# Optimization experiments

Measured on AMD Instinct MI355X. Metric: run time of the kernel, lower is better.

Reference implementation:

```python
import jax, jax.numpy as jnp
import numpy as np

B, S, V, D, H, C, NH = 8, 512, 32000, 768, 768, 9, 8
DH = D // NH


def setup_inputs() -> dict:
    key = jax.random.key(0)
    ks = list(jax.random.split(key, 24))
    it = iter(ks)

    def w(shape, s=0.02):
        return jax.random.normal(next(it), shape, jnp.float32) * s

    return {
        "input_ids": jax.random.randint(next(it), (B, S), 0, V, dtype=jnp.int32),
        "labels": jax.random.randint(next(it), (B, S), 0, C, dtype=jnp.int32),
        "emb_table": w((V, D), 1.0),
        "hw_Wh": w((D, D)),
        "hw_bh": jnp.zeros((D,), jnp.float32),
        "hw_Wt": w((D, D)),
        "hw_bt": jnp.zeros((D,), jnp.float32),
        "in_proj_w": w((3 * D, D)),
        "in_proj_b": jnp.zeros((3 * D,), jnp.float32),
        "out_proj_w": w((D, D)),
        "out_proj_b": jnp.zeros((D,), jnp.float32),
        "lstm0_Wih": w((2, 4 * H, D)),
        "lstm0_Whh": w((2, 4 * H, H)),
        "lstm0_b": jnp.zeros((2, 4 * H), jnp.float32),
        "lstm1_Wih": w((2, 4 * H, 2 * H)),
        "lstm1_Whh": w((2, 4 * H, H)),
        "lstm1_b": jnp.zeros((2, 4 * H), jnp.float32),
        "fc_W": w((C, 2 * H)),
        "fc_b": jnp.zeros((C,), jnp.float32),
        "crf_start": w((C,), 0.1),
        "crf_end": w((C,), 0.1),
        "crf_trans": w((C, C), 0.1),
    }


def _lstm_dir(x, Wih, Whh, b, reverse):
    # x: [B,S,in] -> outputs [B,S,H]; PyTorch gate order i,f,g,o
    xt = x.transpose(1, 0, 2)  # [S,B,in]
    h0 = jnp.zeros((x.shape[0], H), x.dtype)

    def step(carry, xt_):
        h, c = carry
        g = xt_ @ Wih.T + h @ Whh.T + b
        i, f, gg, o = jnp.split(g, 4, axis=-1)
        c = jax.nn.sigmoid(f) * c + jax.nn.sigmoid(i) * jnp.tanh(gg)
        h = jax.nn.sigmoid(o) * jnp.tanh(c)
        return (h, c), h

    _, hs = jax.lax.scan(step, (h0, h0), xt, reverse=reverse)
    return hs.transpose(1, 0, 2)


def _bilstm_layer(x, Wih, Whh, b):
    fwd = _lstm_dir(x, Wih[0], Whh[0], b[0], False)
    bwd = _lstm_dir(x, Wih[1], Whh[1], b[1], True)
    return jnp.concatenate([fwd, bwd], axis=-1)


def _emissions(input_ids, emb_table, hw_Wh, hw_bh, hw_Wt, hw_bt,
               in_proj_w, in_proj_b, out_proj_w, out_proj_b,
               lstm0_Wih, lstm0_Whh, lstm0_b, lstm1_Wih, lstm1_Whh, lstm1_b,
               fc_W, fc_b):
    x = emb_table[input_ids]  # [B,S,D]
    # Highway (1 layer, relu)
    hh = jax.nn.relu(x @ hw_Wh.T + hw_bh)
    t = jax.nn.sigmoid(x @ hw_Wt.T + hw_bt)
    x = t * hh + (1.0 - t) * x
    # Multi-head self-attention
    qkv = x @ in_proj_w.T + in_proj_b
    q, k, v = jnp.split(qkv, 3, axis=-1)
    hd = lambda a: a.reshape(B, S, NH, DH).transpose(0, 2, 1, 3)  # [B,NH,S,DH]
    q, k, v = hd(q), hd(k), hd(v)
    att = jax.nn.softmax(jnp.einsum('bhqd,bhkd->bhqk', q, k) / np.float32(np.sqrt(DH)), axis=-1)
    o = jnp.einsum('bhqk,bhkd->bhqd', att, v).transpose(0, 2, 1, 3).reshape(B, S, D)
    x = o @ out_proj_w.T + out_proj_b
    # 2-layer BiLSTM (inference: dropout off)
    x = _bilstm_layer(x, lstm0_Wih, lstm0_Whh, lstm0_b)
    x = _bilstm_layer(x, lstm1_Wih, lstm1_Whh, lstm1_b)
    return x @ fc_W.T + fc_b  # [B,S,C]


def _crf_nll(emissions, tags, crf_start, crf_end, crf_trans):
    # full mask (labels==-100 replaced by 0 before mask built), reduction='sum'
    em_t = emissions.transpose(1, 0, 2)  # [S,B,C]
    num = crf_start[tags[:, 0]] + crf_end[tags[:, -1]]
    num = num + jnp.take_along_axis(emissions, tags[..., None], axis=-1)[..., 0].sum(-1)
    num = num + crf_trans[tags[:, :-1], tags[:, 1:]].sum(-1)
    a0 = crf_start + em_t[0]  # [B,C]

    def fstep(a, em):
        a = jax.scipy.special.logsumexp(a[:, :, None] + crf_trans[None], axis=1) + em
        return a, None

    aT, _ = jax.lax.scan(fstep, a0, em_t[1:])
    logZ = jax.scipy.special.logsumexp(aT + crf_end, axis=-1)
    return -(num - logZ).sum()


def _viterbi(emissions, crf_start, crf_end, crf_trans):
    em_t = emissions.transpose(1, 0, 2)  # [S,B,C]
    s0 = crf_start + em_t[0]

    def vstep(s, em):
        sc = s[:, :, None] + crf_trans[None]  # [B,C_prev,C_next]
        return jnp.max(sc, axis=1) + em, jnp.argmax(sc, axis=1)

    sT, bps = jax.lax.scan(vstep, s0, em_t[1:])  # bps: [S-1,B,C]
    last = jnp.argmax(sT + crf_end, axis=-1)  # [B]

    def bstep(tag, bp):
        prev = jnp.take_along_axis(bp, tag[:, None], axis=1)[:, 0]
        return prev, prev

    _, path = jax.lax.scan(bstep, last, bps, reverse=True)  # [S-1,B]
    return jnp.concatenate([path, last[None]], axis=0).transpose(1, 0)  # [B,S]


def reference(input_ids, labels, emb_table, hw_Wh, hw_bh, hw_Wt, hw_bt,
              in_proj_w, in_proj_b, out_proj_w, out_proj_b,
              lstm0_Wih, lstm0_Whh, lstm0_b, lstm1_Wih, lstm1_Whh, lstm1_b,
              fc_W, fc_b, crf_start, crf_end, crf_trans):
    emissions = _emissions(input_ids, emb_table, hw_Wh, hw_bh, hw_Wt, hw_bt,
                           in_proj_w, in_proj_b, out_proj_w, out_proj_b,
                           lstm0_Wih, lstm0_Whh, lstm0_b,
                           lstm1_Wih, lstm1_Whh, lstm1_b, fc_W, fc_b)
    loss = _crf_nll(emissions, labels, crf_start, crf_end, crf_trans)
    decode = _viterbi(emissions, crf_start, crf_end, crf_trans)
    return loss, decode
```

## Files before the change

### kernel.cpp

```cpp
#include <hip/hip_runtime.h>
#include <cstdint>

#define B_   8
#define S_   512
#define D_   768
#define C_   9
#define BS_  4096

typedef unsigned long long u64;

__global__ __launch_bounds__(192) void k_embed(const int* __restrict__ ids,
                                               const float* __restrict__ emb,
                                               float* __restrict__ x) {
  int row = blockIdx.x;
  int id = ids[row];
  const float4* src = (const float4*)(emb + (size_t)id * D_);
  float4* dst = (float4*)(x + (size_t)row * D_);
  dst[threadIdx.x] = src[threadIdx.x];
}

#define GIDX(k, m) ((k)*144 + (m) + (((m) >> 5) << 2))

__global__ __launch_bounds__(256) void k_gemm(const float* __restrict__ A,
                                              const float* __restrict__ W,
                                              const float* __restrict__ bias,
                                              float* __restrict__ C,
                                              int M, int N, int K, int act, int mode) {
  __shared__ float As[2304];
  __shared__ float Bs[2304];
  int nwg = gridDim.x * gridDim.y;
  int lin = blockIdx.y * gridDim.x + blockIdx.x;
  int cpx = nwg >> 3;
  int swz = (lin & 7) * cpx + (lin >> 3);
  int bxs = swz % gridDim.x, bys = swz / gridDim.x;
  int bm0 = bys * 128, bn0 = bxs * 128;
  int tid = threadIdx.x;
  int tm = tid >> 4, tn = tid & 15;
  float acc[8][8];
#pragma unroll
  for (int i = 0; i < 8; ++i)
#pragma unroll
    for (int j = 0; j < 8; ++j) acc[i][j] = 0.f;

  for (int k0 = 0; k0 < K; k0 += 16) {
    __syncthreads();
#pragma unroll
    for (int j = 0; j < 2; ++j) {
      int f4 = tid + j * 256;
      int r = f4 >> 2;
      int kq = (f4 & 3) * 4;
      float4 va = *(const float4*)(A + (size_t)(bm0 + r) * K + k0 + kq);
      As[GIDX(kq + 0, r)] = va.x; As[GIDX(kq + 1, r)] = va.y;
      As[GIDX(kq + 2, r)] = va.z; As[GIDX(kq + 3, r)] = va.w;
      float4 vb = *(const float4*)(W + (size_t)(bn0 + r) * K + k0 + kq);
      Bs[GIDX(kq + 0, r)] = vb.x; Bs[GIDX(kq + 1, r)] = vb.y;
      Bs[GIDX(kq + 2, r)] = vb.z; Bs[GIDX(kq + 3, r)] = vb.w;
    }
    __syncthreads();
#pragma unroll
    for (int kk = 0; kk < 16; ++kk) {
      float a[8], b[8];
      *(float4*)&a[0] = *(const float4*)&As[GIDX(kk, tm * 8)];
      *(float4*)&a[4] = *(const float4*)&As[GIDX(kk, tm * 8 + 4)];
      *(float4*)&b[0] = *(const float4*)&Bs[GIDX(kk, tn * 8)];
      *(float4*)&b[4] = *(const float4*)&Bs[GIDX(kk, tn * 8 + 4)];
#pragma unroll
      for (int i = 0; i < 8; ++i)
#pragma unroll
        for (int j = 0; j < 8; ++j) acc[i][j] += a[i] * b[j];
    }
  }

  float bv[8];
#pragma unroll
  for (int j = 0; j < 8; ++j) bv[j] = bias[bn0 + tn * 8 + j];
#pragma unroll
  for (int i = 0; i < 8; ++i) {
    int row = bm0 + tm * 8 + i;
    float o[8];
#pragma unroll
    for (int j = 0; j < 8; ++j) {
      float v = acc[i][j] + bv[j];
      if (act == 1) v = fmaxf(v, 0.f);
      else if (act == 2) v = 1.f / (1.f + expf(-v));
      o[j] = v;
    }
    if (mode == 0) {
      float* cp = C + (size_t)row * N + bn0 + tn * 8;
      *(float4*)cp = make_float4(o[0], o[1], o[2], o[3]);
      *(float4*)(cp + 4) = make_float4(o[4], o[5], o[6], o[7]);
    } else {
      int bb = row >> 9, t = row & 511;
#pragma unroll
      for (int j = 0; j < 8; ++j) {
        unsigned n = bn0 + tn * 8 + j;
        unsigned dir = n / 3072u;
        unsigned n2 = n - dir * 3072u;
        unsigned g = n2 / 768u;
        unsigned rem = n2 - g * 768u;
        unsigned grp = rem >> 3, u = rem & 7;
        C[(((size_t)(dir * 512 + t) * 96 + grp) << 8) + u * 32 + g * 8 + bb] = o[j];
      }
    }
  }
}

__global__ __launch_bounds__(256) void k_highway(float* __restrict__ x,
                                                 const float* __restrict__ hh,
                                                 const float* __restrict__ tt) {
  const int n4 = BS_ * D_ / 4;
  for (int i = blockIdx.x * 256 + threadIdx.x; i < n4; i += gridDim.x * 256) {
    float4 xv = ((const float4*)x)[i];
    float4 hv = ((const float4*)hh)[i];
    float4 tv = ((const float4*)tt)[i];
    xv.x = tv.x * hv.x + (1.f - tv.x) * xv.x;
    xv.y = tv.y * hv.y + (1.f - tv.y) * xv.y;
    xv.z = tv.z * hv.z + (1.f - tv.z) * xv.z;
    xv.w = tv.w * hv.w + (1.f - tv.w) * xv.w;
    ((float4*)x)[i] = xv;
  }
}

__global__ __launch_bounds__(256) void k_attn(const float* __restrict__ qkv,
                                              float* __restrict__ out) {
  __shared__ float Qs[16 * 100];
  __shared__ float Ks[32 * 101];
  __shared__ float Ps[16 * 513];
  int bh = blockIdx.x;
  int b = bh >> 3, h = bh & 7;
  int q0 = blockIdx.y * 16;
  int tid = threadIdx.x;
  const float scale = 0.10206207261596577f;

  const float* qb = qkv + (size_t)(b * 512 + q0) * 2304 + h * 96;
  for (int i = tid; i < 16 * 96; i += 256) {
    int r = i / 96, c = i - r * 96;
    Qs[r * 100 + c] = qb[(size_t)r * 2304 + c];
  }
  int qi = tid >> 4, kseg = tid & 15;

  for (int kt = 0; kt < 16; ++kt) {
    __syncthreads();
    const float* kb = qkv + (size_t)(b * 512 + kt * 32) * 2304 + 768 + h * 96;
    for (int i = tid; i < 32 * 96; i += 256) {
      int r = i / 96, c = i - r * 96;
      Ks[r * 101 + c] = kb[(size_t)r * 2304 + c];
    }
    __syncthreads();
    int kj0 = kseg * 2;
    float s0 = 0.f, s1 = 0.f;
    const float* qrow = &Qs[qi * 100];
    const float* k0p = &Ks[kj0 * 101];
    const float* k1p = &Ks[(kj0 + 1) * 101];
#pragma unroll 8
    for (int d = 0; d < 96; ++d) {
      float qv = qrow[d];
      s0 += qv * k0p[d];
      s1 += qv * k1p[d];
    }
    Ps[qi * 513 + kt * 32 + kj0] = s0 * scale;
    Ps[qi * 513 + kt * 32 + kj0 + 1] = s1 * scale;
  }
  __syncthreads();

  {
    float m = -1e30f;
    for (int j = 0; j < 32; ++j) m = fmaxf(m, Ps[qi * 513 + kseg + j * 16]);
    m = fmaxf(m, __shfl_xor(m, 1)); m = fmaxf(m, __shfl_xor(m, 2));
    m = fmaxf(m, __shfl_xor(m, 4)); m = fmaxf(m, __shfl_xor(m, 8));
    float sum = 0.f;
    for (int j = 0; j < 32; ++j) {
      int idx = qi * 513 + kseg + j * 16;
      float e = expf(Ps[idx] - m);
      Ps[idx] = e;
      sum += e;
    }
    sum += __shfl_xor(sum, 1); sum += __shfl_xor(sum, 2);
    sum += __shfl_xor(sum, 4); sum += __shfl_xor(sum, 8);
    float inv = 1.f / sum;
    for (int j = 0; j < 32; ++j) Ps[qi * 513 + kseg + j * 16] *= inv;
  }

  float acc[6] = {0.f, 0.f, 0.f, 0.f, 0.f, 0.f};
  int d0 = kseg * 6;
  for (int kt = 0; kt < 16; ++kt) {
    __syncthreads();
    const float* vb = qkv + (size_t)(b * 512 + kt * 32) * 2304 + 1536 + h * 96;
    for (int i = tid; i < 32 * 96; i += 256) {
      int r = i / 96, c = i - r * 96;
      Ks[r * 101 + c] = vb[(size_t)r * 2304 + c];
    }
    __syncthreads();
#pragma unroll 4
    for (int kj = 0; kj < 32; ++kj) {
      float p = Ps[qi * 513 + kt * 32 + kj];
      const float* vrow = &Ks[kj * 101 + d0];
#pragma unroll
      for (int u = 0; u < 6; ++u) acc[u] += p * vrow[u];
    }
  }
  float* ob = out + (size_t)(b * 512 + q0 + qi) * 768 + h * 96 + d0;
#pragma unroll
  for (int u = 0; u < 6; ++u) ob[u] = acc[u];
}

#define NWGD 96
__global__ __launch_bounds__(256, 1) void k_lstm(const float* __restrict__ gates,
                                                 const float* __restrict__ Whh,
                                                 float* __restrict__ hbuf,
                                                 float* __restrict__ hs,
                                                 int* __restrict__ flags) {
  __shared__ float hlds[8 * 772];
  int tid = threadIdx.x;
  int wg = blockIdx.x;
  int dir = wg / NWGD;
  int grp = wg % NWGD;
  int rg = tid >> 5;
  int ks = tid & 31;

  float4 w4[4][6];
#pragma unroll
  for (int j = 0; j < 4; ++j) {
    const float* wp = Whh + ((size_t)dir * 3072 + j * 768 + grp * 8 + rg) * 768 + ks * 4;
#pragma unroll
    for (int jj = 0; jj < 6; ++jj)
      w4[j][jj] = *(const float4*)(wp + jj * 128);
  }

  float* hb = hbuf + (size_t)dir * 2 * 6144;
  const float* gbase = gates + (size_t)dir * 512 * 24576 + grp * 256 + tid;
  const float* hp = hlds + ks * 4;
  float cst = 0.f;

  for (int step = 0; step < 512; ++step) {
    int t = dir ? (511 - step) : step;
    float gqv = gbase[(size_t)t * 24576];

#pragma unroll
    for (int i = 0; i < 3; ++i) {
      int idx = i * 256 + tid;
      int b2 = idx / 96;
      int kq = (idx - b2 * 96) * 8;
      const u64* src = (const u64*)(hb + (step & 1) * 6144 + b2 * 768 + kq);
      u64 lo  = __hip_atomic_load(src + 0, __ATOMIC_RELAXED, __HIP_MEMORY_SCOPE_AGENT);
      u64 hi  = __hip_atomic_load(src + 1, __ATOMIC_RELAXED, __HIP_MEMORY_SCOPE_AGENT);
      u64 lo2 = __hip_atomic_load(src + 2, __ATOMIC_RELAXED, __HIP_MEMORY_SCOPE_AGENT);
      u64 hi2 = __hip_atomic_load(src + 3, __ATOMIC_RELAXED, __HIP_MEMORY_SCOPE_AGENT);
      float* dst = &hlds[b2 * 772 + kq];
      *(u64*)(dst + 0) = lo;
      *(u64*)(dst + 2) = hi;
      *(u64*)(dst + 4) = lo2;
      *(u64*)(dst + 6) = hi2;
    }
    __syncthreads();

    float v[32];
#pragma unroll
    for (int i = 0; i < 32; ++i) v[i] = 0.f;
#pragma unroll
    for (int jj = 0; jj < 6; ++jj) {
#pragma unroll
      for (int b2 = 0; b2 < 8; ++b2) {
        float4 hv = *(const float4*)(hp + b2 * 772 + jj * 128);
#pragma unroll
        for (int j = 0; j < 4; ++j) {
          float4 w = w4[j][jj];
          v[j * 8 + b2] = fmaf(w.x, hv.x, v[j * 8 + b2]);
          v[j * 8 + b2] = fmaf(w.y, hv.y, v[j * 8 + b2]);
          v[j * 8 + b2] = fmaf(w.z, hv.z, v[j * 8 + b2]);
          v[j * 8 + b2] = fmaf(w.w, hv.w, v[j * 8 + b2]);
        }
      }
    }

    {
      bool hi = (ks & 16) != 0;
#pragma unroll
      for (int i = 0; i < 16; ++i) {
        float keep = hi ? v[i + 16] : v[i];
        float send = hi ? v[i] : v[i + 16];
        v[i] = keep + __shfl_xor(send, 16);
      }
    }
    {
      bool hi = (ks & 8) != 0;
#pragma unroll
      for (int i = 0; i < 8; ++i) {
        float keep = hi ? v[i + 8] : v[i];
        float send = hi ? v[i] : v[i + 8];
        v[i] = keep + __shfl_xor(send, 8);
      }
    }
    {
      bool hi = (ks & 4) != 0;
#pragma unroll
      for (int i = 0; i < 4; ++i) {
        float keep = hi ? v[i + 4] : v[i];
        float send = hi ? v[i] : v[i + 4];
        v[i] = keep + __shfl_xor(send, 4);
      }
    }
    {
      bool hi = (ks & 2) != 0;
#pragma unroll
      for (int i = 0; i < 2; ++i) {
        float keep = hi ? v[i + 2] : v[i];
        float send = hi ? v[i] : v[i + 2];
        v[i] = keep + __shfl_xor(send, 2);
      }
    }
    {
      bool hi = (ks & 1) != 0;
      float keep = hi ? v[1] : v[0];
      float send = hi ? v[0] : v[1];
      v[0] = keep + __shfl_xor(send, 1);
    }

    float gv = v[0] + gqv;
    float gf = __shfl_down(gv, 8);
    float gg = __shfl_down(gv, 16);
    float go = __shfl_down(gv, 24);
    float hnew = 0.f;
    if (ks < 8) {
      float i_ = 1.f / (1.f + expf(-gv));
      float f_ = 1.f / (1.f + expf(-gf));
      float ci = tanhf(gg);
      float o_ = 1.f / (1.f + expf(-go));
      cst = f_ * cst + i_ * ci;
      hnew = o_ * tanhf(cst);
      __hip_atomic_store(hb + (size_t)((step + 1) & 1) * 6144 + ks * 768 + grp * 8 + rg,
                         hnew, __ATOMIC_RELAXED, __HIP_MEMORY_SCOPE_AGENT);
    }

    __syncthreads();
    if (tid == 0)
      __hip_atomic_store(&flags[wg * 32], step + 1, __ATOMIC_RELAXED, __HIP_MEMORY_SCOPE_AGENT);
    if (ks < 8)
      hs[((size_t)(ks * 512 + t)) * 1536 + dir * 768 + grp * 8 + rg] = hnew;
    if (tid < NWGD) {
      const int* fp = &flags[(dir * NWGD + tid) * 32];
      while (__hip_atomic_load(fp, __ATOMIC_RELAXED, __HIP_MEMORY_SCOPE_AGENT) <= step)
        __builtin_amdgcn_s_sleep(2);
    }
    __syncthreads();
  }
}

__global__ __launch_bounds__(256) void k_fc(const float* __restrict__ A,
                                            const float* __restrict__ Wf,
                                            const float* __restrict__ bf,
                                            float* __restrict__ out) {
  __shared__ float Wl[9 * 1536];
  int tid = threadIdx.x;
  for (int i = tid; i < 9 * 1536; i += 256) Wl[i] = Wf[i];
  __syncthreads();
  int lane = tid & 63, wv = tid >> 6;
  int row = blockIdx.x * 4 + wv;
  const float* a = A + (size_t)row * 1536;
  float acc[9];
#pragma unroll
  for (int c = 0; c < 9; ++c) acc[c] = 0.f;
  for (int i = 0; i < 24; ++i) {
    float av = a[lane + i * 64];
#pragma unroll
    for (int c = 0; c < 9; ++c) acc[c] += av * Wl[c * 1536 + lane + i * 64];
  }
#pragma unroll
  for (int c = 0; c < 9; ++c) {
#pragma unroll
    for (int m = 1; m < 64; m <<= 1) acc[c] += __shfl_xor(acc[c], m);
  }
  if (lane == 0) {
#pragma unroll
    for (int c = 0; c < 9; ++c) out[(size_t)row * 9 + c] = acc[c] + bf[c];
  }
}

__global__ __launch_bounds__(512) void k_crf(const float* __restrict__ em,
                                             const int* __restrict__ labels,
                                             const float* __restrict__ cs,
                                             const float* __restrict__ ce,
                                             const float* __restrict__ ct,
                                             float* __restrict__ out) {
  __shared__ float trans_s[81];
  __shared__ unsigned char bps[8][511][12];
  __shared__ float partres[16];
  int tid = threadIdx.x;
  int b = tid >> 6;
  int lane = tid & 63;
  bool act = lane < 9;
  if (tid < 81) trans_s[tid] = ct[tid];
  __syncthreads();

  float tcol[9];
#pragma unroll
  for (int cp = 0; cp < 9; ++cp) tcol[cp] = act ? trans_s[cp * 9 + lane] : 0.f;

  float a_ = -1e30f, v_ = -1e30f;
  if (act) {
    float e0 = em[((size_t)b * 512) * 9 + lane];
    a_ = cs[lane] + e0;
    v_ = a_;
  }

  float e = act ? em[((size_t)b * 512 + 1) * 9 + lane] : 0.f;
  for (int t = 1; t < 512; ++t) {
    float e_nxt = 0.f;
    if (act && t < 511) e_nxt = em[((size_t)b * 512 + t + 1) * 9 + lane];
    float m = -1e30f, vm = -1e30f;
    int bp = 0;
    float xs[9];
#pragma unroll
    for (int cp = 0; cp < 9; ++cp) {
      float ap = __shfl(a_, cp);
      float vp = __shfl(v_, cp);
      float x = ap + tcol[cp];
      xs[cp] = x;
      m = fmaxf(m, x);
      float y = vp + tcol[cp];
      if (y > vm) { vm = y; bp = cp; }
    }
    float ssum = 0.f;
#pragma unroll
    for (int cp = 0; cp < 9; ++cp) ssum += expf(xs[cp] - m);
    if (act) {
      a_ = m + logf(ssum) + e;
      v_ = vm + e;
      bps[b][t - 1][lane] = (unsigned char)bp;
    }
    e = e_nxt;
  }

  float fin = act ? a_ + ce[lane] : -1e30f;
  float vfin = act ? v_ + ce[lane] : -1e30f;
  float m2 = fin;
  m2 = fmaxf(m2, __shfl_xor(m2, 1)); m2 = fmaxf(m2, __shfl_xor(m2, 2));
  m2 = fmaxf(m2, __shfl_xor(m2, 4)); m2 = fmaxf(m2, __shfl_xor(m2, 8));
  float s2 = expf(fin - m2);
  s2 += __shfl_xor(s2, 1); s2 += __shfl_xor(s2, 2);
  s2 += __shfl_xor(s2, 4); s2 += __shfl_xor(s2, 8);
  float logZ = m2 + logf(s2);

  float bv = vfin; int bi = lane;
#pragma unroll
  for (int s = 1; s < 16; s <<= 1) {
    float ov = __shfl_xor(bv, s);
    int oi = __shfl_xor(bi, s);
    if (ov > bv || (ov == bv && oi < bi)) { bv = ov; bi = oi; }
  }

  float np = 0.f;
  for (int t = lane; t < 512; t += 64) {
    int tg = labels[b * 512 + t];
    np += em[((size_t)b * 512 + t) * 9 + tg];
    if (t < 511) np += trans_s[tg * 9 + labels[b * 512 + t + 1]];
  }
#pragma unroll
  for (int s = 1; s < 64; s <<= 1) np += __shfl_xor(np, s);

  if (lane == 0) {
    np += cs[labels[b * 512]] + ce[labels[b * 512 + 511]];
    partres[b] = np;
    partres[8 + b] = logZ;
    out[1 + b * 512 + 511] = (float)bi;
    int tg = bi;
    for (int t = 510; t >= 0; --t) {
      tg = bps[b][t][tg];
      out[1 + b * 512 + t] = (float)tg;
    }
  }
  __syncthreads();
  if (tid == 0) {
    float acc = 0.f;
#pragma unroll
    for (int b2 = 0; b2 < 8; ++b2) acc += partres[b2] - partres[8 + b2];
    out[0] = -acc;
  }
}

extern "C" void kernel_launch(void* const* d_in, const int* in_sizes, int n_in,
                              void* d_out, int out_size, void* d_ws, size_t ws_size,
                              hipStream_t stream) {
  (void)in_sizes; (void)n_in; (void)out_size; (void)ws_size;
  const int*   ids    = (const int*)d_in[0];
  const int*   labels = (const int*)d_in[1];
  const float* emb    = (const float*)d_in[2];
  const float* hwWh   = (const float*)d_in[3];
  const float* hwbh   = (const float*)d_in[4];
  const float* hwWt   = (const float*)d_in[5];
  const float* hwbt   = (const float*)d_in[6];
  const float* ipw    = (const float*)d_in[7];
  const float* ipb    = (const float*)d_in[8];
  const float* opw    = (const float*)d_in[9];
  const float* opb    = (const float*)d_in[10];
  const float* l0Wih  = (const float*)d_in[11];
  const float* l0Whh  = (const float*)d_in[12];
  const float* l0b    = (const float*)d_in[13];
  const float* l1Wih  = (const float*)d_in[14];
  const float* l1Whh  = (const float*)d_in[15];
  const float* l1b    = (const float*)d_in[16];
  const float* fcW    = (const float*)d_in[17];
  const float* fcb    = (const float*)d_in[18];
  const float* cs     = (const float*)d_in[19];
  const float* ce     = (const float*)d_in[20];
  const float* ct     = (const float*)d_in[21];

  float* ws   = (float*)d_ws;
  float* x0   = ws;
  float* gbuf = ws + 3145728;
  float* hh   = gbuf;
  float* tt   = gbuf + 3145728;
  float* qkv  = gbuf + 6291456;
  float* x1   = ws + 28311552;
  float* hs0  = ws + 31457280;
  float* hs1  = ws + 37748736;
  float* em   = ws + 44040192;
  float* hbuf = ws + 44077056;
  int*   flags = (int*)(ws + 44101632);

  dim3 g768(6, 32), g2304(18, 32), g6144(48, 32);

  k_embed<<<BS_, 192, 0, stream>>>(ids, emb, x0);
  k_gemm<<<g768, 256, 0, stream>>>(x0, hwWh, hwbh, hh, BS_, 768, 768, 1, 0);
  k_gemm<<<g768, 256, 0, stream>>>(x0, hwWt, hwbt, tt, BS_, 768, 768, 2, 0);
  k_highway<<<768, 256, 0, stream>>>(x0, hh, tt);
  k_gemm<<<g2304, 256, 0, stream>>>(x0, ipw, ipb, qkv, BS_, 2304, 768, 0, 0);
  k_attn<<<dim3(64, 32), 256, 0, stream>>>(qkv, x0);
  k_gemm<<<g768, 256, 0, stream>>>(x0, opw, opb, x1, BS_, 768, 768, 0, 0);

  k_gemm<<<g6144, 256, 0, stream>>>(x1, l0Wih, l0b, gbuf, BS_, 6144, 768, 0, 1);
  hipMemsetAsync(hbuf, 0, (24576 + 192 * 32) * sizeof(float), stream);
  k_lstm<<<192, 256, 0, stream>>>(gbuf, l0Whh, hbuf, hs0, flags);

  k_gemm<<<g6144, 256, 0, stream>>>(hs0, l1Wih, l1b, gbuf, BS_, 6144, 1536, 0, 1);
  hipMemsetAsync(hbuf, 0, (24576 + 192 * 32) * sizeof(float), stream);
  k_lstm<<<192, 256, 0, stream>>>(gbuf, l1Whh, hbuf, hs1, flags);

  k_fc<<<1024, 256, 0, stream>>>(hs1, fcW, fcb, em);
  k_crf<<<1, 512, 0, stream>>>(em, labels, cs, ce, ct, (float*)d_out);
}
```

Baseline: 8.094 ms.

## Compute LSTM input-gate GEMMs with split-bf16 MFMA instead of FP32 SIMT

Activations and weights are converted into interleaved hi/lo bf16 planes, so a bf16 MFMA GEMM over 3K (hi*hi, hi*lo, lo*hi) approximates FP32 products for both LSTM input projections. The output is scattered into the same gate layout the recurrence kernel expects. The aim is to replace slow FP32 FMA throughput with matrix-core throughput. In exchange it adds conversion passes and extra workspace, and it depends on the workspace being large enough; otherwise it falls back to the old kernel.

```diff
diff --git a/kernel.cpp b/kernel.cpp
--- a/kernel.cpp
+++ b/kernel.cpp
@@ -1,4 +1,5 @@
 #include <hip/hip_runtime.h>
+#include <hip/hip_bf16.h>
 #include <cstdint>
 
 #define B_   8
@@ -8,6 +9,9 @@
 #define BS_  4096
 
 typedef unsigned long long u64;
+typedef unsigned short ushort_t;
+typedef short bf16x8 __attribute__((ext_vector_type(8)));
+typedef float f32x4 __attribute__((ext_vector_type(4)));
 
 __global__ __launch_bounds__(192) void k_embed(const int* __restrict__ ids,
                                                const float* __restrict__ emb,
@@ -105,6 +109,110 @@
   }
 }
 
+__device__ inline ushort_t f2bf_bits(float x) {
+  __hip_bfloat16 h = __float2bfloat16(x);
+  return __builtin_bit_cast(ushort_t, h);
+}
+__device__ inline float bf2f(ushort_t b) {
+  return __bfloat162float(__builtin_bit_cast(__hip_bfloat16, b));
+}
+
+__global__ __launch_bounds__(256) void k_cvt(const float* __restrict__ src,
+                                             ushort_t* __restrict__ dst,
+                                             int K, int total4, int mode) {
+  int kq4 = K >> 2;
+  for (int idx = blockIdx.x * 256 + threadIdx.x; idx < total4; idx += gridDim.x * 256) {
+    int m = idx / kq4;
+    int kq = (idx - m * kq4) * 4;
+    float4 v = *(const float4*)(src + (size_t)m * K + kq);
+    ushort4 hi, lo;
+    hi.x = f2bf_bits(v.x); lo.x = f2bf_bits(v.x - bf2f(hi.x));
+    hi.y = f2bf_bits(v.y); lo.y = f2bf_bits(v.y - bf2f(hi.y));
+    hi.z = f2bf_bits(v.z); lo.z = f2bf_bits(v.z - bf2f(hi.z));
+    hi.w = f2bf_bits(v.w); lo.w = f2bf_bits(v.w - bf2f(hi.w));
+    ushort_t* base = dst + (size_t)m * 3 * K + kq;
+    *(ushort4*)(base)         = hi;
+    *(ushort4*)(base + K)     = mode ? hi : lo;
+    *(ushort4*)(base + 2 * K) = mode ? lo : hi;
+  }
+}
+
+__global__ __launch_bounds__(256) void k_gates16(const ushort_t* __restrict__ A,
+                                                 const ushort_t* __restrict__ W,
+                                                 const float* __restrict__ bias,
+                                                 float* __restrict__ C,
+                                                 int Kp) {
+  __shared__ ushort_t Asb[128 * 64];
+  __shared__ ushort_t Bsb[128 * 64];
+  int nwg = gridDim.x * gridDim.y;
+  int lin = blockIdx.y * gridDim.x + blockIdx.x;
+  int cpx = nwg >> 3;
+  int swz = (lin & 7) * cpx + (lin >> 3);
+  int bn0 = (swz % gridDim.x) * 128, bm0 = (swz / gridDim.x) * 128;
+  int tid = threadIdx.x;
+  int w = tid >> 6, lane = tid & 63;
+  int lr = lane & 15, lq = lane >> 4;
+  int srow = tid >> 1, shalf = tid & 1;
+
+  f32x4 acc[2][8];
+#pragma unroll
+  for (int i = 0; i < 2; ++i)
+#pragma unroll
+    for (int j = 0; j < 8; ++j) acc[i][j] = (f32x4){0.f, 0.f, 0.f, 0.f};
+
+  const ushort_t* Ap = A + (size_t)(bm0 + srow) * Kp + shalf * 32;
+  const ushort_t* Wp = W + (size_t)(bn0 + srow) * Kp + shalf * 32;
+  int s7 = srow & 7;
+
+  for (int k0 = 0; k0 < Kp; k0 += 64) {
+    __syncthreads();
+#pragma unroll
+    for (int i = 0; i < 4; ++i) {
+      int c = shalf * 4 + i;
+      int cs = c ^ s7;
+      *(uint4*)&Asb[srow * 64 + cs * 8] = *(const uint4*)(Ap + k0 + i * 8);
+      *(uint4*)&Bsb[srow * 64 + cs * 8] = *(const uint4*)(Wp + k0 + i * 8);
+    }
+    __syncthreads();
+#pragma unroll
+    for (int kf = 0; kf < 2; ++kf) {
+      int c = kf * 4 + lq;
+      int rowA0 = w * 32 + lr;
+      int rowA1 = w * 32 + 16 + lr;
+      bf16x8 a0 = *(const bf16x8*)&Asb[rowA0 * 64 + (c ^ (rowA0 & 7)) * 8];
+      bf16x8 a1 = *(const bf16x8*)&Asb[rowA1 * 64 + (c ^ (rowA1 & 7)) * 8];
+#pragma unroll
+      for (int ns = 0; ns < 8; ++ns) {
+        int rowB = ns * 16 + lr;
+        bf16x8 b = *(const bf16x8*)&Bsb[rowB * 64 + (c ^ (rowB & 7)) * 8];
+        acc[0][ns] = __builtin_amdgcn_mfma_f32_16x16x32_bf16(a0, b, acc[0][ns], 0, 0, 0);
+        acc[1][ns] = __builtin_amdgcn_mfma_f32_16x16x32_bf16(a1, b, acc[1][ns], 0, 0, 0);
+      }
+    }
+  }
+
+#pragma unroll
+  for (int ns = 0; ns < 8; ++ns) {
+    unsigned n = bn0 + ns * 16 + lr;
+    unsigned dir = n / 3072u;
+    unsigned n2 = n - dir * 3072u;
+    unsigned g = n2 / 768u;
+    unsigned rem = n2 - g * 768u;
+    unsigned grp = rem >> 3, u = rem & 7;
+    float bv = bias[n];
+#pragma unroll
+    for (int ms = 0; ms < 2; ++ms) {
+#pragma unroll
+      for (int r = 0; r < 4; ++r) {
+        int m = bm0 + w * 32 + ms * 16 + lq * 4 + r;
+        int bb = m >> 9, t = m & 511;
+        C[(((size_t)(dir * 512 + t) * 96 + grp) << 8) + u * 32 + g * 8 + bb] =
+            acc[ms][ns][r] + bv;
+      }
+    }
+  }
+}
+
 __global__ __launch_bounds__(256) void k_highway(float* __restrict__ x,
                                                  const float* __restrict__ hh,
                                                  const float* __restrict__ tt) {
@@ -481,7 +589,7 @@
 extern "C" void kernel_launch(void* const* d_in, const int* in_sizes, int n_in,
                               void* d_out, int out_size, void* d_ws, size_t ws_size,
                               hipStream_t stream) {
-  (void)in_sizes; (void)n_in; (void)out_size; (void)ws_size;
+  (void)in_sizes; (void)n_in; (void)out_size;
   const int*   ids    = (const int*)d_in[0];
   const int*   labels = (const int*)d_in[1];
   const float* emb    = (const float*)d_in[2];
@@ -517,6 +625,10 @@
   float* em   = ws + 44040192;
   float* hbuf = ws + 44077056;
   int*   flags = (int*)(ws + 44101632);
+  ushort_t* bfA = (ushort_t*)(ws + 44107776);
+  ushort_t* bfW = (ushort_t*)(ws + 44107776 + 9437184);
+  const size_t ws_need = (44107776ull + 9437184ull + 14155776ull) * 4ull;
+  bool bf16path = (ws_size >= ws_need);
 
   dim3 g768(6, 32), g2304(18, 32), g6144(48, 32);
 
@@ -528,11 +640,23 @@
   k_attn<<<dim3(64, 32), 256, 0, stream>>>(qkv, x0);
   k_gemm<<<g768, 256, 0, stream>>>(x0, opw, opb, x1, BS_, 768, 768, 0, 0);
 
-  k_gemm<<<g6144, 256, 0, stream>>>(x1, l0Wih, l0b, gbuf, BS_, 6144, 768, 0, 1);
+  if (bf16path) {
+    k_cvt<<<2048, 256, 0, stream>>>(x1, bfA, 768, BS_ * 768 / 4, 0);
+    k_cvt<<<2048, 256, 0, stream>>>(l0Wih, bfW, 768, 6144 * 768 / 4, 1);
+    k_gates16<<<g6144, 256, 0, stream>>>(bfA, bfW, l0b, gbuf, 2304);
+  } else {
+    k_gemm<<<g6144, 256, 0, stream>>>(x1, l0Wih, l0b, gbuf, BS_, 6144, 768, 0, 1);
+  }
   hipMemsetAsync(hbuf, 0, (24576 + 192 * 32) * sizeof(float), stream);
   k_lstm<<<192, 256, 0, stream>>>(gbuf, l0Whh, hbuf, hs0, flags);
 
-  k_gemm<<<g6144, 256, 0, stream>>>(hs0, l1Wih, l1b, gbuf, BS_, 6144, 1536, 0, 1);
+  if (bf16path) {
+    k_cvt<<<2048, 256, 0, stream>>>(hs0, bfA, 1536, BS_ * 1536 / 4, 0);
+    k_cvt<<<4096, 256, 0, stream>>>(l1Wih, bfW, 1536, 6144 * 1536 / 4, 1);
+    k_gates16<<<g6144, 256, 0, stream>>>(bfA, bfW, l1b, gbuf, 4608);
+  } else {
+    k_gemm<<<g6144, 256, 0, stream>>>(hs0, l1Wih, l1b, gbuf, BS_, 6144, 1536, 0, 1);
+  }
   hipMemsetAsync(hbuf, 0, (24576 + 192 * 32) * sizeof(float), stream);
   k_lstm<<<192, 256, 0, stream>>>(gbuf, l1Whh, hbuf, hs1, flags);
 
```

Result: faster. 7.465 ms (-7.8%).
